# Optimization experiments

Measured on AMD Instinct MI355X. Metric: run time of the kernel, lower is better.

The kernel has to match this reference:

```python
import jax, jax.numpy as jnp
import numpy as np

B, T, D_MODEL = 2, 8192, 2048
H, H_KV, D_HEAD = 16, 8, 128
M_LAND, RANK = 64, 64
N_ITER = 6
STD = 0.02


def setup_inputs() -> dict:
    key = jax.random.key(0)
    ks = jax.random.split(key, 7)
    return {
        "x": jax.random.normal(ks[0], (B, T, D_MODEL), jnp.float32),
        "Wq": jax.random.normal(ks[1], (D_MODEL, H * D_HEAD), jnp.float32) * STD,
        "Wk": jax.random.normal(ks[2], (D_MODEL, H_KV * D_HEAD), jnp.float32) * STD,
        "Wv": jax.random.normal(ks[3], (D_MODEL, H_KV * D_HEAD), jnp.float32) * STD,
        "Wo": jax.random.normal(ks[4], (H * D_HEAD, D_MODEL), jnp.float32) * STD,
        "Wkp1": jax.random.normal(ks[5], (D_HEAD, RANK), jnp.float32) * STD,
        "Wkp2": jax.random.normal(ks[6], (RANK, D_HEAD), jnp.float32) * STD,
    }


def _iterative_pinv(A, n_iter=N_ITER):
    # A: (B, H, m, m); Schulz iteration Z <- 2Z - Z A Z
    norm_1 = jnp.max(jnp.sum(jnp.abs(A), axis=-2), axis=-1)
    norm_inf = jnp.max(jnp.sum(jnp.abs(A), axis=-1), axis=-1)
    v = 1.0 / jnp.clip(norm_1 * norm_inf, 1e-7)
    Z = jnp.swapaxes(A, -1, -2) * v[..., None, None]
    for _ in range(n_iter):
        Z = 2.0 * Z - Z @ A @ Z
    return Z


def reference(x, Wq, Wk, Wv, Wo, Wkp1, Wkp2):
    n_rep = H // H_KV
    # projections -> (B, H, T, d)
    q = (x @ Wq).reshape(B, T, H, D_HEAD).transpose(0, 2, 1, 3)
    k = (x @ Wk).reshape(B, T, H_KV, D_HEAD).transpose(0, 2, 1, 3)
    v = (x @ Wv).reshape(B, T, H_KV, D_HEAD).transpose(0, 2, 1, 3)
    k = jnp.repeat(k, n_rep, axis=1)  # GQA repeat_kv
    v = jnp.repeat(v, n_rep, axis=1)

    m = min(M_LAND, T)
    scale = 1.0 / np.sqrt(D_HEAD).astype(np.float32)
    stride = max(T // m, 1)
    idx = jnp.arange(0, T, stride)[:m]
    q_land = q[:, :, idx, :]
    k_land = k[:, :, idx, :]
    kernel_proj = lambda z: z + jax.nn.silu(z @ Wkp1) @ Wkp2
    q_land = kernel_proj(q_land)
    k_land = kernel_proj(k_land)

    K_qm = jax.nn.softmax(jnp.einsum('bhtd,bhmd->bhtm', q, k_land) * scale, axis=-1)
    K_mm = jax.nn.softmax(jnp.einsum('bhmd,bhnd->bhmn', q_land, k_land) * scale, axis=-1)
    K_mk = jax.nn.softmax(jnp.einsum('bhmd,bhtd->bhmt', q_land, k) * scale, axis=-1)
    K_mm_inv = _iterative_pinv(K_mm)

    # associativity-reordered (same math, avoids dense (T,T) intermediate)
    out = K_qm @ (K_mm_inv @ (K_mk @ v))  # (B, H, T, d)
    out = out.transpose(0, 2, 1, 3).reshape(B, T, H * D_HEAD)
    return out @ Wo
```

## Files before the change

kernel.cpp:

```cpp
#include <hip/hip_runtime.h>


#define B_ 2
#define T_ 8192
#define DM 2048
#define H_ 16
#define DH 128
#define NIT 6

typedef unsigned short u16;
typedef __attribute__((ext_vector_type(8))) short bf16x8;
typedef __attribute__((ext_vector_type(4))) float f32x4;
typedef __attribute__((ext_vector_type(4))) unsigned short u16x4;

__device__ __forceinline__ u16 f2bf(float f) {
    unsigned u = __float_as_uint(f);
    u += 0x7FFFu + ((u >> 16) & 1u);
    return (u16)(u >> 16);
}

__device__ __forceinline__ void async16(const void* g, void* l) {
    __builtin_amdgcn_global_load_lds((const __attribute__((address_space(1))) void*)g,
                                     (__attribute__((address_space(3))) void*)l,
                                     16, 0, 0);
}

__global__ void cvt_x_kernel(const float* __restrict__ x, u16* __restrict__ xb, int n4) {
    int i = blockIdx.x * blockDim.x + threadIdx.x;
    int stride = gridDim.x * blockDim.x;
    for (; i < n4; i += stride) {
        float4 v = ((const float4*)x)[i];
        u16x4 o;
        o.x = f2bf(v.x); o.y = f2bf(v.y); o.z = f2bf(v.z); o.w = f2bf(v.w);
        ((u16x4*)xb)[i] = o;
    }
}

__global__ void tconv_kernel(const float* __restrict__ src, u16* __restrict__ dst, int R, int C) {
    __shared__ float tl[32][33];
    int c0 = blockIdx.x * 32, r0 = blockIdx.y * 32;
    int tx = threadIdx.x, ty = threadIdx.y;
    #pragma unroll
    for (int i = ty; i < 32; i += 8)
        tl[i][tx] = src[(size_t)(r0 + i) * C + c0 + tx];
    __syncthreads();
    #pragma unroll
    for (int i = ty; i < 32; i += 8)
        dst[(size_t)(c0 + i) * R + r0 + tx] = f2bf(tl[tx][i]);
}

__global__ void tv_kernel(const u16* __restrict__ v, u16* __restrict__ vT) {
    int bg = blockIdx.z;
    const u16* src = v + (size_t)(bg >> 3) * T_ * 1024 + (bg & 7) * DH;
    u16* dst = vT + (size_t)bg * DH * T_;
    __shared__ u16 tl[32][33];
    int t0 = blockIdx.x * 32, d0 = blockIdx.y * 32;
    int tx = threadIdx.x, ty = threadIdx.y;
    #pragma unroll
    for (int i = ty; i < 32; i += 8)
        tl[i][tx] = src[(size_t)(t0 + i) * 1024 + d0 + tx];
    __syncthreads();
    #pragma unroll
    for (int i = ty; i < 32; i += 8)
        dst[(size_t)(d0 + i) * T_ + t0 + tx] = tl[tx][i];
}


#define BAR()   __builtin_amdgcn_s_barrier()
#define SB0()   __builtin_amdgcn_sched_barrier(0)
#define LGKM0() do { asm volatile("s_waitcnt lgkmcnt(0)" ::: "memory"); SB0(); } while (0)
#define VM6()   do { asm volatile("s_waitcnt vmcnt(6)" ::: "memory"); } while (0)

#define RD_A(S, BUF, H) do {                                                  \
    const char* _p = lA_rd + (BUF) * 32768 + (H) * 16384;                     \
    _Pragma("unroll") for (int _m = 0; _m < 4; ++_m) {                        \
        Af[S][_m][0] = *(const bf16x8*)(_p + _m * 2048 + kswz0);              \
        Af[S][_m][1] = *(const bf16x8*)(_p + _m * 2048 + kswz1);              \
    }                                                                         \
} while (0)

#define RD_B(S, BUF, H) do {                                                  \
    const char* _p = lB_rd + (BUF) * 32768 + (H) * 16384;                     \
    _Pragma("unroll") for (int _n = 0; _n < 2; ++_n) {                        \
        Bf[S][_n][0] = *(const bf16x8*)(_p + _n * 2048 + kswz0);              \
        Bf[S][_n][1] = *(const bf16x8*)(_p + _n * 2048 + kswz1);              \
    }                                                                         \
} while (0)

#define ST_A(BUF, H, T) do {                                                  \
    const u16* _g = gA + (size_t)(H) * 64 * K + (size_t)(T) * 64;             \
    char* _l = lsAst + (BUF) * 32768 + (H) * 16384;                           \
    async16(_g, _l);                                                          \
    async16(_g + (size_t)128 * K, _l + 8192);                                 \
} while (0)

#define ST_B(BUF, H, T) do {                                                  \
    const u16* _g = gB + (size_t)(H) * 32 * K + (size_t)(T) * 64;             \
    char* _l = lsBst + (BUF) * 32768 + (H) * 16384;                           \
    async16(_g, _l);                                                          \
    async16(_g + (size_t)128 * K, _l + 8192);                                 \
} while (0)

#define MFMA_Q(AM, BN)                                                        \
    _Pragma("unroll") for (int _m = 0; _m < 4; ++_m)                          \
    _Pragma("unroll") for (int _n = 0; _n < 2; ++_n)                          \
    _Pragma("unroll") for (int _k = 0; _k < 2; ++_k)                          \
        acc[(AM) * 4 + _m][(BN) * 2 + _n] =                                   \
            __builtin_amdgcn_mfma_f32_16x16x32_bf16(                          \
                Af[AM][_m][_k], Bf[BN][_n][_k],                               \
                acc[(AM) * 4 + _m][(BN) * 2 + _n], 0, 0, 0);

template<int MODE>
__global__ __launch_bounds__(512) void gemm256_kernel(
    const u16* __restrict__ A, const u16* __restrict__ Bt,
    u16* __restrict__ oq, u16* __restrict__ ok, u16* __restrict__ ov,
    float* __restrict__ of, int K, int nxt)
{
    __shared__ u16 lsA[2][2][128][64];
    __shared__ u16 lsB[2][2][128][64];

    const int tid  = threadIdx.x;
    const int lane = tid & 63;
    const int w    = tid >> 6;
    const int wr   = w >> 2, wc = w & 3;
    const int fr   = lane & 15, fg = lane >> 4;

    const int cpx = (int)gridDim.x >> 3;
    const int bid = ((int)blockIdx.x & 7) * cpx + ((int)blockIdx.x >> 3);
    const int bx = bid % nxt, by = bid / nxt;
    const long R0 = (long)by * 256, C0 = (long)bx * 256;

    const int sr = tid >> 3;
    const int sc = tid & 7;
    const int koff = ((sc ^ (sr & 7)) * 8);
    const u16* gA = A  + (R0 + sr) * (size_t)K + koff;
    const u16* gB = Bt + (C0 + (sr >> 5) * 64 + (sr & 31)) * (size_t)K + koff;
    char* lsAst = (char*)lsA + w * 1024;
    char* lsBst = (char*)lsB + w * 1024;

    const int kswz0 = (0 * 64 + fg * 16) ^ ((fr & 7) << 4);
    const int kswz1 = (1 * 64 + fg * 16) ^ ((fr & 7) << 4);
    const char* lA_rd = (const char*)lsA + (wr * 64 + fr) * 128;
    const char* lB_rd = (const char*)lsB + (wc * 32 + fr) * 128;

    f32x4 acc[8][4] = {};
    bf16x8 Af[2][4][2], Bf[2][2][2];

    const int NT = K >> 6;

    ST_A(0, 0, 0); ST_B(0, 0, 0); ST_B(0, 1, 0); ST_A(0, 1, 0);
    ST_A(1, 0, 1); ST_B(1, 0, 1); ST_B(1, 1, 1);
    VM6();
    BAR(); SB0();

    for (int t = 0; t < NT; ++t) {
        const int buf = t & 1;
        RD_A(0, buf, 0);
        if (t + 1 < NT) ST_A(buf ^ 1, 1, t + 1);
        BAR(); LGKM0();
        __builtin_amdgcn_s_setprio(1);
        if (t > 0) { MFMA_Q(1, 1); }
        __builtin_amdgcn_s_setprio(0);
        BAR(); SB0();
        RD_B(0, buf, 0);
        if (t + 2 < NT) ST_A(buf, 0, t + 2);
        BAR(); LGKM0();
        __builtin_amdgcn_s_setprio(1);
        MFMA_Q(0, 0);
        __builtin_amdgcn_s_setprio(0);
        BAR(); SB0();
        RD_B(1, buf, 1);
        if (t + 2 < NT) ST_B(buf, 0, t + 2);
        BAR(); LGKM0();
        __builtin_amdgcn_s_setprio(1);
        MFMA_Q(0, 1);
        __builtin_amdgcn_s_setprio(0);
        BAR(); SB0();
        RD_A(1, buf, 1);
        if (t + 2 < NT) ST_B(buf, 1, t + 2);
        VM6();
        BAR(); LGKM0();
        __builtin_amdgcn_s_setprio(1);
        MFMA_Q(1, 0);
        __builtin_amdgcn_s_setprio(0);
        BAR(); SB0();
    }
    MFMA_Q(1, 1);

    const long rb0 = R0 + wr * 128 + fg * 4;
    const int  cb0 = (int)C0 + wc * 64 + fr;
    #pragma unroll
    for (int mi = 0; mi < 8; ++mi)
        #pragma unroll
        for (int ni = 0; ni < 4; ++ni)
            #pragma unroll
            for (int rr = 0; rr < 4; ++rr) {
                long rg = rb0 + mi * 16 + rr;
                int  nn = cb0 + ni * 16;
                float val = acc[mi][ni][rr];
                if (MODE == 0) {
                    u16 o = f2bf(val);
                    if (nn < 2048)      oq[rg * 2048 + nn] = o;
                    else if (nn < 3072) ok[rg * 1024 + (nn - 2048)] = o;
                    else                ov[rg * 1024 + (nn - 3072)] = o;
                } else {
                    of[rg * 2048 + nn] = val;
                }
            }
}

__global__ __launch_bounds__(256) void land_gemm_kernel(
    const float* __restrict__ x, const float* __restrict__ Wq,
    const float* __restrict__ Wk, float* __restrict__ land_raw)
{
    __shared__ float xs[128][36];
    __shared__ float ws[32][132];
    const int tid = threadIdx.x;
    const int n0 = blockIdx.x * 128;
    const int tm0 = (tid >> 4) * 8, tn0 = (tid & 15) * 8;
    float accr[8][8] = {};

    for (int it = 0; it < 8; ++it) {
        const int k0 = blockIdx.y * 256 + it * 32;
        __syncthreads();
        for (int idx = tid * 4; idx < 4096; idx += 1024) {
            int r = idx >> 5, c = idx & 31;
            *(float4*)&xs[r][c] =
                *(const float4*)&x[((size_t)(r >> 6) * T_ + (r & 63) * 128) * DM + k0 + c];
        }
        if (n0 < 2048) {
            for (int idx = tid * 4; idx < 4096; idx += 1024) {
                int k = idx >> 7, c = idx & 127;
                *(float4*)&ws[k][c] = *(const float4*)&Wq[(size_t)(k0 + k) * 2048 + n0 + c];
            }
        } else {
            for (int idx = tid * 4; idx < 4096; idx += 1024) {
                int k = idx >> 7, c = idx & 127;
                *(float4*)&ws[k][c] = *(const float4*)&Wk[(size_t)(k0 + k) * 1024 + (n0 - 2048) + c];
            }
        }
        __syncthreads();
        for (int k = 0; k < 32; ++k) {
            float a[8];
            #pragma unroll
            for (int i = 0; i < 8; ++i) a[i] = xs[tm0 + i][k];
            f32x4 b0 = *(const f32x4*)&ws[k][tn0];
            f32x4 b1 = *(const f32x4*)&ws[k][tn0 + 4];
            #pragma unroll
            for (int i = 0; i < 8; ++i) {
                accr[i][0] += a[i] * b0[0]; accr[i][1] += a[i] * b0[1];
                accr[i][2] += a[i] * b0[2]; accr[i][3] += a[i] * b0[3];
                accr[i][4] += a[i] * b1[0]; accr[i][5] += a[i] * b1[1];
                accr[i][6] += a[i] * b1[2]; accr[i][7] += a[i] * b1[3];
            }
        }
    }
    for (int i = 0; i < 8; ++i)
        for (int j = 0; j < 8; ++j)
            atomicAdd(&land_raw[(size_t)(tm0 + i) * 3072 + n0 + tn0 + j], accr[i][j]);
}

__global__ void proj_kernel(const float* __restrict__ land_raw,
    const float* __restrict__ Wkp1, const float* __restrict__ Wkp2,
    float* __restrict__ qlf, float* __restrict__ klf,
    u16* __restrict__ qlb, u16* __restrict__ klb)
{
    const int bid = blockIdx.x;
    const int type = bid & 1;
    const int m = (bid >> 1) & 63;
    const int bh = bid >> 7;
    const int b = bh >> 4, h = bh & 15;
    const int lane = threadIdx.x;
    const int lm = b * 64 + m;
    const float* src = (type == 0)
        ? land_raw + (size_t)lm * 3072 + h * 128
        : land_raw + (size_t)lm * 3072 + 2048 + (h >> 1) * 128;
    __shared__ float zb[128];
    __shared__ float sb[64];
    float z0 = src[lane], z1 = src[lane + 64];
    zb[lane] = z0; zb[lane + 64] = z1;
    __syncthreads();
    float hsum = 0.f;
    #pragma unroll 4
    for (int d = 0; d < 128; ++d) hsum += zb[d] * Wkp1[d * 64 + lane];
    sb[lane] = hsum / (1.f + __expf(-hsum));
    __syncthreads();
    float o0 = z0, o1 = z1;
    #pragma unroll 4
    for (int j = 0; j < 64; ++j) {
        float sj = sb[j];
        o0 += sj * Wkp2[j * 128 + lane];
        o1 += sj * Wkp2[j * 128 + lane + 64];
    }
    size_t oidx = ((size_t)bh * 64 + m) * 128 + lane;
    float* fo = (type == 0) ? qlf : klf;
    u16*   bo = (type == 0) ? qlb : klb;
    fo[oidx] = o0; fo[oidx + 64] = o1;
    bo[oidx] = f2bf(o0); bo[oidx + 64] = f2bf(o1);
}

__global__ __launch_bounds__(256) void pinv_kernel(
    const float* __restrict__ qlf, const float* __restrict__ klf, float* __restrict__ inv)
{
    const int bh = blockIdx.x;
    const int tid = threadIdx.x;
    const int m = tid >> 2, nq = tid & 3, n0b = nq * 16;
    __shared__ float Am[64][68];
    __shared__ float Z[64][68];
    __shared__ float Wm[64][68];
    __shared__ float cs[64], rsn[64];
    __shared__ float vsc;
    const float scale = 0.08838834764831845f;

    float accr[16] = {};
    const float* qrow = qlf + ((size_t)bh * 64 + m) * 128;
    for (int dc = 0; dc < 4; ++dc) {
        f32x4 qv[8];
        #pragma unroll
        for (int u = 0; u < 8; ++u) qv[u] = *(const f32x4*)&qrow[dc * 32 + u * 4];
        for (int nn = 0; nn < 16; ++nn) {
            const float* kp = klf + ((size_t)bh * 64 + n0b + nn) * 128 + dc * 32;
            float s = 0.f;
            #pragma unroll
            for (int u = 0; u < 8; ++u) {
                f32x4 kv = *(const f32x4*)&kp[u * 4];
                s += qv[u][0]*kv[0] + qv[u][1]*kv[1] + qv[u][2]*kv[2] + qv[u][3]*kv[3];
            }
            accr[nn] += s;
        }
    }
    float rsum = 0.f;
    #pragma unroll
    for (int nn = 0; nn < 16; ++nn) { accr[nn] = __expf(accr[nn] * scale); rsum += accr[nn]; }
    rsum += __shfl_xor(rsum, 1);
    rsum += __shfl_xor(rsum, 2);
    float rinv = 1.f / rsum;
    #pragma unroll
    for (int nn = 0; nn < 16; ++nn) Am[m][n0b + nn] = accr[nn] * rinv;
    __syncthreads();
    if (tid < 64) {
        float s = 0.f;
        for (int i = 0; i < 64; ++i) s += Am[i][tid];
        cs[tid] = s;
    } else if (tid < 128) {
        int r = tid - 64; float s = 0.f;
        for (int j = 0; j < 64; ++j) s += Am[r][j];
        rsn[r] = s;
    }
    __syncthreads();
    if (tid == 0) {
        float n1 = 0.f, ni = 0.f;
        for (int i = 0; i < 64; ++i) { n1 = fmaxf(n1, cs[i]); ni = fmaxf(ni, rsn[i]); }
        float pr = n1 * ni; if (pr < 1e-7f) pr = 1e-7f;
        vsc = 1.f / pr;
    }
    __syncthreads();
    {
        float v = vsc;
        for (int u = 0; u < 16; ++u) {
            int idx = tid * 16 + u;
            Z[idx >> 6][idx & 63] = Am[idx & 63][idx >> 6] * v;
        }
    }
    for (int it = 0; it < NIT; ++it) {
        __syncthreads();
        float wacc[16] = {};
        for (int k = 0; k < 64; ++k) {
            float a = Am[m][k];
            f32x4 z0 = *(const f32x4*)&Z[k][n0b];
            f32x4 z1 = *(const f32x4*)&Z[k][n0b + 4];
            f32x4 z2 = *(const f32x4*)&Z[k][n0b + 8];
            f32x4 z3 = *(const f32x4*)&Z[k][n0b + 12];
            #pragma unroll
            for (int u = 0; u < 4; ++u) {
                wacc[u]      += a * z0[u];
                wacc[u + 4]  += a * z1[u];
                wacc[u + 8]  += a * z2[u];
                wacc[u + 12] += a * z3[u];
            }
        }
        #pragma unroll
        for (int nn = 0; nn < 16; ++nn) Wm[m][n0b + nn] = wacc[nn];
        __syncthreads();
        float zacc[16] = {};
        for (int k = 0; k < 64; ++k) {
            float zk = Z[m][k];
            f32x4 w0 = *(const f32x4*)&Wm[k][n0b];
            f32x4 w1 = *(const f32x4*)&Wm[k][n0b + 4];
            f32x4 w2 = *(const f32x4*)&Wm[k][n0b + 8];
            f32x4 w3 = *(const f32x4*)&Wm[k][n0b + 12];
            #pragma unroll
            for (int u = 0; u < 4; ++u) {
                zacc[u]      += zk * w0[u];
                zacc[u + 4]  += zk * w1[u];
                zacc[u + 8]  += zk * w2[u];
                zacc[u + 12] += zk * w3[u];
            }
        }
        #pragma unroll
        for (int nn = 0; nn < 16; ++nn) zacc[nn] = 2.f * Z[m][n0b + nn] - zacc[nn];
        __syncthreads();
        #pragma unroll
        for (int nn = 0; nn < 16; ++nn) Z[m][n0b + nn] = zacc[nn];
    }
    __syncthreads();
    for (int u = 0; u < 16; ++u) {
        int idx = tid * 16 + u;
        inv[(size_t)bh * 4096 + idx] = Z[idx >> 6][idx & 63];
    }
}

__global__ __launch_bounds__(64) void attn_mk_kernel(
    const u16* __restrict__ qlb, const u16* __restrict__ kb,
    const u16* __restrict__ vT, float* __restrict__ agg_acc, float* __restrict__ agg_sum)
{
    const int bid = blockIdx.x;
    const int chunk = bid & 31;
    const int bh = bid >> 5;
    const int b = bh >> 4, h = bh & 15, g = h >> 1;
    const int t0 = chunk * 256;
    const int lane = threadIdx.x;
    const int fr = lane & 15, fg = lane >> 4;
    const float scale = 0.08838834764831845f;
    __shared__ u16 P[64][264];

    float rst[4][4] = {};
    const u16* qbase = qlb + ((size_t)bh * 64 + fr) * 128 + fg * 8;

    for (int sc = 0; sc < 4; ++sc) {
        f32x4 S[4][4] = {};
        const u16* kbase = kb + ((size_t)(b * T_ + t0 + sc * 64 + fr)) * 1024 + g * 128 + fg * 8;
        #pragma unroll
        for (int ks = 0; ks < 4; ++ks) {
            bf16x8 a[4], bv[4];
            #pragma unroll
            for (int i = 0; i < 4; ++i) a[i] = *(const bf16x8*)(qbase + (size_t)i * 16 * 128 + ks * 32);
            #pragma unroll
            for (int j = 0; j < 4; ++j) bv[j] = *(const bf16x8*)(kbase + (size_t)j * 16 * 1024 + ks * 32);
            #pragma unroll
            for (int i = 0; i < 4; ++i)
                #pragma unroll
                for (int j = 0; j < 4; ++j)
                    S[i][j] = __builtin_amdgcn_mfma_f32_16x16x32_bf16(a[i], bv[j], S[i][j], 0, 0, 0);
        }
        #pragma unroll
        for (int i = 0; i < 4; ++i)
            #pragma unroll
            for (int j = 0; j < 4; ++j)
                #pragma unroll
                for (int r = 0; r < 4; ++r) {
                    float pv = __expf(S[i][j][r] * scale);
                    rst[i][r] += pv;
                    P[i * 16 + fg * 4 + r][sc * 64 + j * 16 + fr] = f2bf(pv);
                }
    }
    __syncthreads();
    #pragma unroll
    for (int i = 0; i < 4; ++i)
        #pragma unroll
        for (int r = 0; r < 4; ++r) {
            float t = rst[i][r];
            t += __shfl_xor(t, 1); t += __shfl_xor(t, 2);
            t += __shfl_xor(t, 4); t += __shfl_xor(t, 8);
            if (fr == 0) atomicAdd(&agg_sum[(size_t)bh * 64 + i * 16 + fg * 4 + r], t);
        }
    const u16* vbase = vT + ((size_t)(b * 8 + g) * 128 + fr) * T_ + t0 + fg * 8;
    #pragma unroll
    for (int dh = 0; dh < 2; ++dh) {
        f32x4 O[4][4] = {};
        #pragma unroll
        for (int ks = 0; ks < 8; ++ks) {
            bf16x8 pa[4], vv[4];
            #pragma unroll
            for (int i = 0; i < 4; ++i) pa[i] = *(const bf16x8*)&P[i * 16 + fr][ks * 32 + fg * 8];
            #pragma unroll
            for (int j = 0; j < 4; ++j) vv[j] = *(const bf16x8*)(vbase + ((size_t)dh * 64 + j * 16) * T_ + ks * 32);
            #pragma unroll
            for (int i = 0; i < 4; ++i)
                #pragma unroll
                for (int j = 0; j < 4; ++j)
                    O[i][j] = __builtin_amdgcn_mfma_f32_16x16x32_bf16(pa[i], vv[j], O[i][j], 0, 0, 0);
        }
        #pragma unroll
        for (int i = 0; i < 4; ++i)
            #pragma unroll
            for (int j = 0; j < 4; ++j)
                #pragma unroll
                for (int r = 0; r < 4; ++r)
                    atomicAdd(&agg_acc[((size_t)bh * 64 + i * 16 + fg * 4 + r) * 128 + dh * 64 + j * 16 + fr],
                              O[i][j][r]);
    }
}

__global__ __launch_bounds__(256) void mid_kernel(
    const float* __restrict__ inv, const float* __restrict__ agg_acc,
    const float* __restrict__ agg_sum, u16* __restrict__ midt)
{
    const int bh = blockIdx.x;
    const int tid = threadIdx.x;
    __shared__ float invl[64][68];
    __shared__ float an[64][129];
    for (int idx = tid; idx < 4096; idx += 256)
        invl[idx >> 6][idx & 63] = inv[(size_t)bh * 4096 + idx];
    for (int idx = tid; idx < 8192; idx += 256) {
        int j = idx >> 7, d = idx & 127;
        an[j][d] = agg_acc[((size_t)bh * 64 + j) * 128 + d] / agg_sum[(size_t)bh * 64 + j];
    }
    __syncthreads();
    const int m = tid >> 2, dq = tid & 3;
    float accv[32] = {};
    for (int j = 0; j < 64; ++j) {
        float a = invl[m][j];
        #pragma unroll
        for (int dd = 0; dd < 32; ++dd)
            accv[dd] += a * an[j][dq * 32 + dd];
    }
    for (int dd = 0; dd < 32; ++dd)
        midt[(size_t)bh * 8192 + (dq * 32 + dd) * 64 + m] = f2bf(accv[dd]);
}

__global__ __launch_bounds__(256) void attn_qm_kernel(
    const u16* __restrict__ qb, const u16* __restrict__ klb,
    const u16* __restrict__ midt, u16* __restrict__ ao)
{
    const int bid = blockIdx.x;
    const int tile = bid & 63;
    const int bh = bid >> 6;
    const int b = bh >> 4, h = bh & 15;
    const int w = threadIdx.x >> 6;
    const int lane = threadIdx.x & 63;
    const int fr = lane & 15, fg = lane >> 4;
    const int trow0 = tile * 128 + w * 32;
    const float scale = 0.08838834764831845f;
    __shared__ u16 Pl[4][32][72];

    f32x4 S[2][4] = {};
    const u16* qbase = qb + ((size_t)(b * T_ + trow0 + fr)) * 2048 + h * 128 + fg * 8;
    const u16* kbase = klb + ((size_t)bh * 64 + fr) * 128 + fg * 8;
    #pragma unroll
    for (int ks = 0; ks < 4; ++ks) {
        bf16x8 a[2], bv[4];
        #pragma unroll
        for (int i = 0; i < 2; ++i) a[i] = *(const bf16x8*)(qbase + (size_t)i * 16 * 2048 + ks * 32);
        #pragma unroll
        for (int j = 0; j < 4; ++j) bv[j] = *(const bf16x8*)(kbase + (size_t)j * 16 * 128 + ks * 32);
        #pragma unroll
        for (int i = 0; i < 2; ++i)
            #pragma unroll
            for (int j = 0; j < 4; ++j)
                S[i][j] = __builtin_amdgcn_mfma_f32_16x16x32_bf16(a[i], bv[j], S[i][j], 0, 0, 0);
    }
    #pragma unroll
    for (int i = 0; i < 2; ++i) {
        float rsv[4] = {0.f, 0.f, 0.f, 0.f};
        #pragma unroll
        for (int j = 0; j < 4; ++j)
            #pragma unroll
            for (int r = 0; r < 4; ++r) {
                float pv = __expf(S[i][j][r] * scale);
                S[i][j][r] = pv;
                rsv[r] += pv;
            }
        #pragma unroll
        for (int r = 0; r < 4; ++r) {
            float t = rsv[r];
            t += __shfl_xor(t, 1); t += __shfl_xor(t, 2);
            t += __shfl_xor(t, 4); t += __shfl_xor(t, 8);
            rsv[r] = 1.f / t;
        }
        #pragma unroll
        for (int j = 0; j < 4; ++j)
            #pragma unroll
            for (int r = 0; r < 4; ++r)
                Pl[w][i * 16 + fg * 4 + r][j * 16 + fr] = f2bf(S[i][j][r] * rsv[r]);
    }
    __syncthreads();
    f32x4 O[2][8] = {};
    const u16* mbase = midt + ((size_t)bh * 128 + fr) * 64 + fg * 8;
    #pragma unroll
    for (int ks = 0; ks < 2; ++ks) {
        bf16x8 pa[2], mb[8];
        #pragma unroll
        for (int i = 0; i < 2; ++i) pa[i] = *(const bf16x8*)&Pl[w][i * 16 + fr][ks * 32 + fg * 8];
        #pragma unroll
        for (int j = 0; j < 8; ++j) mb[j] = *(const bf16x8*)(mbase + (size_t)j * 16 * 64 + ks * 32);
        #pragma unroll
        for (int i = 0; i < 2; ++i)
            #pragma unroll
            for (int j = 0; j < 8; ++j)
                O[i][j] = __builtin_amdgcn_mfma_f32_16x16x32_bf16(pa[i], mb[j], O[i][j], 0, 0, 0);
    }
    u16* obase = ao + ((size_t)(b * T_ + trow0 + fg * 4)) * 2048 + h * 128 + fr;
    #pragma unroll
    for (int i = 0; i < 2; ++i)
        #pragma unroll
        for (int j = 0; j < 8; ++j)
            #pragma unroll
            for (int r = 0; r < 4; ++r)
                obase[((size_t)i * 16 + r) * 2048 + j * 16] = f2bf(O[i][j][r]);
}

extern "C" void kernel_launch(void* const* d_in, const int* in_sizes, int n_in,
                              void* d_out, int out_size, void* d_ws, size_t ws_size,
                              hipStream_t stream)
{
    const float* x    = (const float*)d_in[0];
    const float* Wq   = (const float*)d_in[1];
    const float* Wk   = (const float*)d_in[2];
    const float* Wv   = (const float*)d_in[3];
    const float* Wo   = (const float*)d_in[4];
    const float* Wkp1 = (const float*)d_in[5];
    const float* Wkp2 = (const float*)d_in[6];
    float* out = (float*)d_out;

    char* p = (char*)d_ws;
    auto alloc = [&](size_t bytes) { char* r = p; p += (bytes + 255) & ~(size_t)255; return r; };
    u16*   x_bf     = (u16*)alloc(67108864);
    u16*   q_bf     = (u16*)alloc(67108864);
    u16*   kv_bf    = (u16*)alloc(67108864);
    u16*   Wcat_t   = (u16*)alloc(16777216);
    float* land_raw = (float*)alloc(1572864);
    float* qlf      = (float*)alloc(2097152);
    float* klf      = (float*)alloc(2097152);
    u16*   qlb      = (u16*)alloc(1048576);
    u16*   klb      = (u16*)alloc(1048576);
    float* invb     = (float*)alloc(524288);
    float* agg_acc  = (float*)alloc(2097152);
    float* agg_sum  = (float*)alloc(32768);
    u16*   midt     = (u16*)alloc(1048576);

    u16* k_bf = kv_bf;
    u16* v_bf = kv_bf + (size_t)16384 * 1024;
    u16* vT       = x_bf;
    u16* attn_out = kv_bf;
    u16* Wo_t     = Wcat_t;

    (void)hipMemsetAsync(land_raw, 0, 1572864, stream);
    (void)hipMemsetAsync(agg_acc, 0, 2097152, stream);
    (void)hipMemsetAsync(agg_sum, 0, 32768, stream);

    cvt_x_kernel<<<2048, 256, 0, stream>>>(x, x_bf, 16384 * 2048 / 4);
    tconv_kernel<<<dim3(64, 64), dim3(32, 8), 0, stream>>>(Wq, Wcat_t, 2048, 2048);
    tconv_kernel<<<dim3(32, 64), dim3(32, 8), 0, stream>>>(Wk, Wcat_t + (size_t)2048 * 2048, 2048, 1024);
    tconv_kernel<<<dim3(32, 64), dim3(32, 8), 0, stream>>>(Wv, Wcat_t + (size_t)3072 * 2048, 2048, 1024);
    gemm256_kernel<0><<<1024, 512, 0, stream>>>(x_bf, Wcat_t, q_bf, k_bf, v_bf, nullptr, 2048, 16);
    land_gemm_kernel<<<dim3(24, 8), 256, 0, stream>>>(x, Wq, Wk, land_raw);
    proj_kernel<<<4096, 64, 0, stream>>>(land_raw, Wkp1, Wkp2, qlf, klf, qlb, klb);
    pinv_kernel<<<32, 256, 0, stream>>>(qlf, klf, invb);
    tv_kernel<<<dim3(256, 4, 16), dim3(32, 8), 0, stream>>>(v_bf, vT);
    attn_mk_kernel<<<1024, 64, 0, stream>>>(qlb, k_bf, vT, agg_acc, agg_sum);
    mid_kernel<<<32, 256, 0, stream>>>(invb, agg_acc, agg_sum, midt);
    tconv_kernel<<<dim3(64, 64), dim3(32, 8), 0, stream>>>(Wo, Wo_t, 2048, 2048);
    attn_qm_kernel<<<2048, 256, 0, stream>>>(q_bf, klb, midt, attn_out);
    gemm256_kernel<1><<<512, 512, 0, stream>>>(attn_out, Wo_t, nullptr, nullptr, nullptr, out, 2048, 8);
}
```

Measured before the change: 1.084 ms.

## Replace float atomics with partial-sum slabs and deterministic reduction kernels

The landmark GEMM now writes per-split partial results into separate slabs, and proj_kernel sums them, instead of atomically adding into a zeroed buffer. attn_mk is split into twice as many 128-token chunks that write per-chunk partial accumulators and sums into the output buffer, used as scratch. A new reduce_mk kernel sums these partials and normalises them before mid_kernel. This removes the three memsets and the contended float atomics, and doubles attn_mk parallelism. In exchange it adds an extra kernel launch and more global traffic for the partial slabs.

```diff
diff --git a/kernel.cpp b/kernel.cpp
--- a/kernel.cpp
+++ b/kernel.cpp
@@ -211,7 +211,7 @@
 
 __global__ __launch_bounds__(256) void land_gemm_kernel(
     const float* __restrict__ x, const float* __restrict__ Wq,
-    const float* __restrict__ Wk, float* __restrict__ land_raw)
+    const float* __restrict__ Wk, float* __restrict__ land_part)
 {
     __shared__ float xs[128][36];
     __shared__ float ws[32][132];
@@ -255,12 +255,13 @@
             }
         }
     }
+    float* o = land_part + (size_t)blockIdx.y * 393216;
     for (int i = 0; i < 8; ++i)
         for (int j = 0; j < 8; ++j)
-            atomicAdd(&land_raw[(size_t)(tm0 + i) * 3072 + n0 + tn0 + j], accr[i][j]);
-}
-
-__global__ void proj_kernel(const float* __restrict__ land_raw,
+            o[(size_t)(tm0 + i) * 3072 + n0 + tn0 + j] = accr[i][j];
+}
+
+__global__ void proj_kernel(const float* __restrict__ land_part,
     const float* __restrict__ Wkp1, const float* __restrict__ Wkp2,
     float* __restrict__ qlf, float* __restrict__ klf,
     u16* __restrict__ qlb, u16* __restrict__ klb)
@@ -272,12 +273,17 @@
     const int b = bh >> 4, h = bh & 15;
     const int lane = threadIdx.x;
     const int lm = b * 64 + m;
-    const float* src = (type == 0)
-        ? land_raw + (size_t)lm * 3072 + h * 128
-        : land_raw + (size_t)lm * 3072 + 2048 + (h >> 1) * 128;
+    const size_t off = (type == 0)
+        ? (size_t)lm * 3072 + h * 128
+        : (size_t)lm * 3072 + 2048 + (h >> 1) * 128;
     __shared__ float zb[128];
     __shared__ float sb[64];
-    float z0 = src[lane], z1 = src[lane + 64];
+    float z0 = 0.f, z1 = 0.f;
+    #pragma unroll
+    for (int s = 0; s < 8; ++s) {
+        z0 += land_part[(size_t)s * 393216 + off + lane];
+        z1 += land_part[(size_t)s * 393216 + off + lane + 64];
+    }
     zb[lane] = z0; zb[lane + 64] = z1;
     __syncthreads();
     float hsum = 0.f;
@@ -412,22 +418,22 @@
 
 __global__ __launch_bounds__(64) void attn_mk_kernel(
     const u16* __restrict__ qlb, const u16* __restrict__ kb,
-    const u16* __restrict__ vT, float* __restrict__ agg_acc, float* __restrict__ agg_sum)
+    const u16* __restrict__ vT, float* __restrict__ pacc, float* __restrict__ psum)
 {
     const int bid = blockIdx.x;
-    const int chunk = bid & 31;
-    const int bh = bid >> 5;
+    const int chunk = bid & 63;
+    const int bh = bid >> 6;
     const int b = bh >> 4, h = bh & 15, g = h >> 1;
-    const int t0 = chunk * 256;
+    const int t0 = chunk * 128;
     const int lane = threadIdx.x;
     const int fr = lane & 15, fg = lane >> 4;
     const float scale = 0.08838834764831845f;
-    __shared__ u16 P[64][264];
+    __shared__ u16 P[64][136];
 
     float rst[4][4] = {};
     const u16* qbase = qlb + ((size_t)bh * 64 + fr) * 128 + fg * 8;
 
-    for (int sc = 0; sc < 4; ++sc) {
+    for (int sc = 0; sc < 2; ++sc) {
         f32x4 S[4][4] = {};
         const u16* kbase = kb + ((size_t)(b * T_ + t0 + sc * 64 + fr)) * 1024 + g * 128 + fg * 8;
         #pragma unroll
@@ -462,14 +468,15 @@
             float t = rst[i][r];
             t += __shfl_xor(t, 1); t += __shfl_xor(t, 2);
             t += __shfl_xor(t, 4); t += __shfl_xor(t, 8);
-            if (fr == 0) atomicAdd(&agg_sum[(size_t)bh * 64 + i * 16 + fg * 4 + r], t);
-        }
+            if (fr == 0) psum[((size_t)chunk * 32 + bh) * 64 + i * 16 + fg * 4 + r] = t;
+        }
+    float* pslab = pacc + (((size_t)chunk * 32 + bh) * 64) * 128;
     const u16* vbase = vT + ((size_t)(b * 8 + g) * 128 + fr) * T_ + t0 + fg * 8;
     #pragma unroll
     for (int dh = 0; dh < 2; ++dh) {
         f32x4 O[4][4] = {};
         #pragma unroll
-        for (int ks = 0; ks < 8; ++ks) {
+        for (int ks = 0; ks < 4; ++ks) {
             bf16x8 pa[4], vv[4];
             #pragma unroll
             for (int i = 0; i < 4; ++i) pa[i] = *(const bf16x8*)&P[i * 16 + fr][ks * 32 + fg * 8];
@@ -487,14 +494,47 @@
             for (int j = 0; j < 4; ++j)
                 #pragma unroll
                 for (int r = 0; r < 4; ++r)
-                    atomicAdd(&agg_acc[((size_t)bh * 64 + i * 16 + fg * 4 + r) * 128 + dh * 64 + j * 16 + fr],
-                              O[i][j][r]);
+                    pslab[(size_t)(i * 16 + fg * 4 + r) * 128 + dh * 64 + j * 16 + fr] = O[i][j][r];
+    }
+}
+
+__global__ __launch_bounds__(256) void reduce_mk_kernel(
+    const float* __restrict__ pacc, const float* __restrict__ psum,
+    float* __restrict__ an)
+{
+    const int bh = blockIdx.x;
+    const int tid = threadIdx.x;
+    __shared__ float ss[64];
+    if (tid < 64) {
+        float s = 0.f;
+        for (int c = 0; c < 64; ++c) s += psum[((size_t)c * 32 + bh) * 64 + tid];
+        ss[tid] = s;
+    }
+    __syncthreads();
+    const int r = tid >> 2;
+    const int d0 = (tid & 3) * 32;
+    f32x4 acc[8] = {};
+    for (int c = 0; c < 64; ++c) {
+        const float* p = pacc + (((size_t)c * 32 + bh) * 64 + r) * 128 + d0;
+        #pragma unroll
+        for (int u = 0; u < 8; ++u) {
+            f32x4 v = *(const f32x4*)(p + u * 4);
+            acc[u][0] += v[0]; acc[u][1] += v[1];
+            acc[u][2] += v[2]; acc[u][3] += v[3];
+        }
+    }
+    const float rinv = 1.f / ss[r];
+    float* o = an + ((size_t)bh * 64 + r) * 128 + d0;
+    #pragma unroll
+    for (int u = 0; u < 8; ++u) {
+        o[u * 4 + 0] = acc[u][0] * rinv; o[u * 4 + 1] = acc[u][1] * rinv;
+        o[u * 4 + 2] = acc[u][2] * rinv; o[u * 4 + 3] = acc[u][3] * rinv;
     }
 }
 
 __global__ __launch_bounds__(256) void mid_kernel(
-    const float* __restrict__ inv, const float* __restrict__ agg_acc,
-    const float* __restrict__ agg_sum, u16* __restrict__ midt)
+    const float* __restrict__ inv, const float* __restrict__ an_g,
+    u16* __restrict__ midt)
 {
     const int bh = blockIdx.x;
     const int tid = threadIdx.x;
@@ -504,7 +544,7 @@
         invl[idx >> 6][idx & 63] = inv[(size_t)bh * 4096 + idx];
     for (int idx = tid; idx < 8192; idx += 256) {
         int j = idx >> 7, d = idx & 127;
-        an[j][d] = agg_acc[((size_t)bh * 64 + j) * 128 + d] / agg_sum[(size_t)bh * 64 + j];
+        an[j][d] = an_g[((size_t)bh * 64 + j) * 128 + d];
     }
     __syncthreads();
     const int m = tid >> 2, dq = tid & 3;
@@ -615,19 +655,18 @@
 
     char* p = (char*)d_ws;
     auto alloc = [&](size_t bytes) { char* r = p; p += (bytes + 255) & ~(size_t)255; return r; };
-    u16*   x_bf     = (u16*)alloc(67108864);
-    u16*   q_bf     = (u16*)alloc(67108864);
-    u16*   kv_bf    = (u16*)alloc(67108864);
-    u16*   Wcat_t   = (u16*)alloc(16777216);
-    float* land_raw = (float*)alloc(1572864);
-    float* qlf      = (float*)alloc(2097152);
-    float* klf      = (float*)alloc(2097152);
-    u16*   qlb      = (u16*)alloc(1048576);
-    u16*   klb      = (u16*)alloc(1048576);
-    float* invb     = (float*)alloc(524288);
-    float* agg_acc  = (float*)alloc(2097152);
-    float* agg_sum  = (float*)alloc(32768);
-    u16*   midt     = (u16*)alloc(1048576);
+    u16*   x_bf      = (u16*)alloc(67108864);
+    u16*   q_bf      = (u16*)alloc(67108864);
+    u16*   kv_bf     = (u16*)alloc(67108864);
+    u16*   Wcat_t    = (u16*)alloc(16777216);
+    float* land_part = (float*)alloc(12582912);
+    float* qlf       = (float*)alloc(2097152);
+    float* klf       = (float*)alloc(2097152);
+    u16*   qlb       = (u16*)alloc(1048576);
+    u16*   klb       = (u16*)alloc(1048576);
+    float* invb      = (float*)alloc(524288);
+    float* an        = (float*)alloc(1048576);
+    u16*   midt      = (u16*)alloc(1048576);
 
     u16* k_bf = kv_bf;
     u16* v_bf = kv_bf + (size_t)16384 * 1024;
@@ -635,21 +674,21 @@
     u16* attn_out = kv_bf;
     u16* Wo_t     = Wcat_t;
 
-    (void)hipMemsetAsync(land_raw, 0, 1572864, stream);
-    (void)hipMemsetAsync(agg_acc, 0, 2097152, stream);
-    (void)hipMemsetAsync(agg_sum, 0, 32768, stream);
+    float* pacc = out;
+    float* psum = out + (size_t)16777216;
 
     cvt_x_kernel<<<2048, 256, 0, stream>>>(x, x_bf, 16384 * 2048 / 4);
     tconv_kernel<<<dim3(64, 64), dim3(32, 8), 0, stream>>>(Wq, Wcat_t, 2048, 2048);
     tconv_kernel<<<dim3(32, 64), dim3(32, 8), 0, stream>>>(Wk, Wcat_t + (size_t)2048 * 2048, 2048, 1024);
     tconv_kernel<<<dim3(32, 64), dim3(32, 8), 0, stream>>>(Wv, Wcat_t + (size_t)3072 * 2048, 2048, 1024);
     gemm256_kernel<0><<<1024, 512, 0, stream>>>(x_bf, Wcat_t, q_bf, k_bf, v_bf, nullptr, 2048, 16);
-    land_gemm_kernel<<<dim3(24, 8), 256, 0, stream>>>(x, Wq, Wk, land_raw);
-    proj_kernel<<<4096, 64, 0, stream>>>(land_raw, Wkp1, Wkp2, qlf, klf, qlb, klb);
+    land_gemm_kernel<<<dim3(24, 8), 256, 0, stream>>>(x, Wq, Wk, land_part);
+    proj_kernel<<<4096, 64, 0, stream>>>(land_part, Wkp1, Wkp2, qlf, klf, qlb, klb);
     pinv_kernel<<<32, 256, 0, stream>>>(qlf, klf, invb);
     tv_kernel<<<dim3(256, 4, 16), dim3(32, 8), 0, stream>>>(v_bf, vT);
-    attn_mk_kernel<<<1024, 64, 0, stream>>>(qlb, k_bf, vT, agg_acc, agg_sum);
-    mid_kernel<<<32, 256, 0, stream>>>(invb, agg_acc, agg_sum, midt);
+    attn_mk_kernel<<<2048, 64, 0, stream>>>(qlb, k_bf, vT, pacc, psum);
+    reduce_mk_kernel<<<32, 256, 0, stream>>>(pacc, psum, an);
+    mid_kernel<<<32, 256, 0, stream>>>(invb, an, midt);
     tconv_kernel<<<dim3(64, 64), dim3(32, 8), 0, stream>>>(Wo, Wo_t, 2048, 2048);
     attn_qm_kernel<<<2048, 256, 0, stream>>>(q_bf, klb, midt, attn_out);
     gemm256_kernel<1><<<512, 512, 0, stream>>>(attn_out, Wo_t, nullptr, nullptr, nullptr, out, 2048, 8);
```

Result: no change. 1.066 ms (-1.7%).
